# Optimization experiments

Measured on AMD Instinct MI355X. Metric: run time of the kernel, lower is better.

The kernel has to match this reference:

```python
import jax, jax.numpy as jnp
import numpy as np

T, B, OBS, H, M1, M2, A = 64, 2048, 48, 256, 512, 256, 12
LOG2PI = float(np.log(2.0 * np.pi))
LOG_STD_MIN, LOG_STD_MAX = -5.0, 2.0
LN_EPS = 1e-5


def _elu(x):
    return jnp.where(x > 0, x, jnp.expm1(x))


def setup_inputs() -> dict:
    key = jax.random.key(0)
    ks = jax.random.split(key, 10)
    s = lambda k, shape, sc=0.05: jax.random.normal(k, shape, jnp.float32) * sc
    return dict(
        x=jax.random.normal(ks[0], (T, B, OBS), jnp.float32),
        done=jax.random.randint(ks[1], (T, B), 0, 2).astype(jnp.int32),
        h0=jnp.zeros((B, H), jnp.float32),
        c0=jnp.zeros((B, H), jnp.float32),
        W_ih=s(ks[2], (4 * H, OBS)),
        W_hh=s(ks[3], (4 * H, H)),
        b_ih=jnp.zeros((4 * H,), jnp.float32),
        b_hh=jnp.zeros((4 * H,), jnp.float32),
        ln_g=jnp.ones((H,), jnp.float32),
        ln_b=jnp.zeros((H,), jnp.float32),
        W1=s(ks[4], (H, M1)),
        b1=jnp.zeros((M1,), jnp.float32),
        W2=s(ks[5], (M1, M2)),
        b2=jnp.zeros((M2,), jnp.float32),
        Wm=s(ks[6], (M2, A), 0.01),
        bm=jnp.zeros((A,), jnp.float32),
        Ws=s(ks[7], (M2, A), 0.01),
        bs=jnp.zeros((A,), jnp.float32),
    )


def reference(x, h0, c0, W_ih, W_hh, b_ih, b_hh, ln_g, ln_b,
              W1, b1, W2, b2, Wm, bm, Ws, bs, done):
    # Precompute input-side gate projections for all timesteps: [T, B, 4H]
    xg = jnp.einsum('tbi,gi->tbg', x, W_ih) + b_ih + b_hh
    keep = 1.0 - done.astype(jnp.float32)  # [T, B]; reset state where done==1

    def step(carry, inp):
        h, c = carry
        xgt, m = inp
        h = h * m[:, None]
        c = c * m[:, None]
        g = xgt + h @ W_hh.T  # [B, 4H], PyTorch gate order i,f,g,o
        i, f, gg, o = jnp.split(g, 4, axis=-1)
        c = jax.nn.sigmoid(f) * c + jax.nn.sigmoid(i) * jnp.tanh(gg)
        h = jax.nn.sigmoid(o) * jnp.tanh(c)
        return (h, c), h

    (_, _), hs = jax.lax.scan(step, (h0, c0), (xg, keep))
    hflat = hs.reshape(T * B, H)

    # LayerNorm
    mu = hflat.mean(-1, keepdims=True)
    var = ((hflat - mu) ** 2).mean(-1, keepdims=True)
    y = (hflat - mu) / jnp.sqrt(var + LN_EPS) * ln_g + ln_b

    # Actor MLP (ELU after every Linear, per build_mlp)
    y = _elu(y @ W1 + b1)
    y = _elu(y @ W2 + b2)

    mean = y @ Wm + bm
    logstd = jnp.clip(y @ Ws + bs, LOG_STD_MIN, LOG_STD_MAX)
    # deterministic action == mean, so (a - mu)^2 / (2 sigma^2) == 0
    logp = (-logstd - 0.5 * LOG2PI).sum(-1)
    ent = (0.5 + 0.5 * LOG2PI + logstd).sum(-1)
    # [T*B, A+2]: action mean, log_prob, entropy
    return jnp.concatenate([mean, logp[:, None], ent[:, None]], axis=-1)
```

## Files before the change

### kernel.cpp

```cpp
#include <hip/hip_runtime.h>
#include <hip/hip_bf16.h>
#include <math.h>

#define T_   64
#define B_   2048
#define OBS_ 48
#define H_   256
#define M1_  512
#define M2_  256
#define A_   12
#define BH_  (B_ * H_)
#define KP_  320
#define GROUPS_  128
#define SLICES_  2
#define RPB_     16

typedef unsigned short u16;
typedef unsigned long long u64;
typedef __attribute__((ext_vector_type(8))) short bf16x8;
typedef __attribute__((ext_vector_type(4))) float f32x4;

static __device__ __forceinline__ u16 f2b(float f) {
    __hip_bfloat16 h = __float2bfloat16(f);
    return *reinterpret_cast<u16*>(&h);
}
static __device__ __forceinline__ float b2f(u16 u) {
    union { unsigned u32v; float f; } v; v.u32v = ((unsigned)u) << 16; return v.f;
}
static __device__ __forceinline__ float sigm(float x) {
    return 1.0f / (1.0f + __expf(-x));
}
static __device__ __forceinline__ float tanh_fast(float x) {
    x = fminf(fmaxf(x, -15.0f), 15.0f);
    float e = __expf(2.0f * x);
    return (e - 1.0f) / (e + 1.0f);
}
static __device__ __forceinline__ float elu(float x) {
    return x > 0.0f ? x : (__expf(x) - 1.0f);
}

__global__ void prep_xpad(const float* __restrict__ x, u16* __restrict__ xpad,
                          unsigned* __restrict__ cnt) {
    if (blockIdx.x == 0 && threadIdx.x < GROUPS_ * SLICES_) cnt[threadIdx.x] = 0;
    const int gid = blockIdx.x * 256 + threadIdx.x;
    const int r = gid >> 3, k0 = (gid & 7) * 8;
    u16 tmp[8];
    if (k0 < OBS_) {
        const float4 f0 = *(const float4*)(x + (size_t)r * OBS_ + k0);
        const float4 f1 = *(const float4*)(x + (size_t)r * OBS_ + k0 + 4);
        tmp[0] = f2b(f0.x); tmp[1] = f2b(f0.y); tmp[2] = f2b(f0.z); tmp[3] = f2b(f0.w);
        tmp[4] = f2b(f1.x); tmp[5] = f2b(f1.y); tmp[6] = f2b(f1.z); tmp[7] = f2b(f1.w);
    } else {
        #pragma unroll
        for (int i = 0; i < 8; ++i) tmp[i] = 0;
    }
    *(uint4*)(xpad + (size_t)gid * 8) = *(uint4*)tmp;
}

__global__ void prep_weights(const float* __restrict__ W_ih, const float* __restrict__ W_hh,
                             const float* __restrict__ W1,  const float* __restrict__ W2,
                             const float* __restrict__ Wm,  const float* __restrict__ Ws,
                             u16* __restrict__ Wcat, u16* __restrict__ W1T,
                             u16* __restrict__ W2T,  u16* __restrict__ WhT) {
    const int b = blockIdx.x, tid = threadIdx.x;
    if (b < 1024) {
        const int s = b >> 9, w = (b >> 6) & 7, g = (b >> 4) & 3, jj = b & 15;
        const int src = g * 256 + s * 128 + w * 16 + jj;
        for (int k = tid; k < KP_; k += 256) {
            float v;
            if (k < OBS_)    v = W_ih[src * OBS_ + k];
            else if (k < 64) v = 0.0f;
            else             v = W_hh[src * H_ + (k - 64)];
            Wcat[b * KP_ + k] = f2b(v);
        }
    } else if (b < 1536) {
        const int n = b - 1024;
        W1T[n * 256 + tid] = f2b(W1[tid * M1_ + n]);
    } else if (b < 1792) {
        const int n = b - 1536;
        W2T[n * 512 + tid]       = f2b(W2[tid * M2_ + n]);
        W2T[n * 512 + tid + 256] = f2b(W2[(tid + 256) * M2_ + n]);
    } else {
        const int n = b - 1792;
        float v = 0.0f;
        if (n < 12)                 v = Wm[tid * A_ + n];
        else if (n >= 16 && n < 28) v = Ws[tid * A_ + (n - 16)];
        WhT[n * 256 + tid] = f2b(v);
    }
}

#define ASM_(row, chunk) (a_sm + (size_t)(row) * 320 + (size_t)(((chunk) ^ ((row) & 7)) << 3))

__global__ __launch_bounds__(512, 2) void lstm_sync2(
    const u16*  __restrict__ xpad,
    const int*  __restrict__ done,
    const float* __restrict__ h0,
    const float* __restrict__ c0,
    u16*        __restrict__ hs,
    const u16*  __restrict__ Wcat,
    const float* __restrict__ b_ih,
    const float* __restrict__ b_hh,
    unsigned*   __restrict__ cnt)
{
    __shared__ u16 a_sm[RPB_ * 320];

    const int tid  = threadIdx.x;
    const int lane = tid & 63;
    const int w    = tid >> 6;
    const int quad = lane >> 4, l16 = lane & 15;
    const int grp  = blockIdx.x >> 1;
    const int s    = blockIdx.x & 1;
    const int b0   = grp * RPB_;
    const int j    = s * 128 + w * 16 + l16;
    const int pc0  = (1 - s) * 128;

    float bsum[4];
    #pragma unroll
    for (int g = 0; g < 4; ++g) bsum[g] = b_ih[g * 256 + j] + b_hh[g * 256 + j];

    float cst[4];
    #pragma unroll
    for (int r = 0; r < 4; ++r) {
        const int row = b0 + quad * 4 + r;
        cst[r] = done[row] ? 0.0f : c0[(size_t)row * H_ + j];
    }

    bf16x8 Bs[4][10];
    #pragma unroll
    for (int g = 0; g < 4; ++g) {
        const u16* wp = Wcat + (size_t)(((s * 8 + w) * 4 + g) * 16 + l16) * KP_ + quad * 8;
        #pragma unroll
        for (int kt = 0; kt < 10; ++kt)
            Bs[g][kt] = *(const bf16x8*)(wp + kt * 32);
    }

    if ((tid & 3) == 0) {
        const int idx = tid >> 2, row = idx >> 3, seg = idx & 7;
        *(uint4*)ASM_(row, seg) =
            *(const uint4*)(xpad + (size_t)(b0 + row) * 64 + seg * 8);
    }
    {
        const int row = tid >> 5, c8 = tid & 31;
        const int dn = done[b0 + row];
        const float* hr = h0 + (size_t)(b0 + row) * H_ + c8 * 8;
        u16 tmp[8];
        #pragma unroll
        for (int e = 0; e < 8; ++e) tmp[e] = dn ? (u16)0 : f2b(hr[e]);
        *(uint4*)ASM_(row, 8 + c8) = *(uint4*)tmp;
    }
    __syncthreads();

    for (int t = 0; t < T_; ++t) {
        f32x4 acc[4];
        #pragma unroll
        for (int g = 0; g < 4; ++g) acc[g] = (f32x4){0, 0, 0, 0};
        #pragma unroll
        for (int kt = 0; kt < 10; ++kt) {
            const bf16x8 af = *(const bf16x8*)ASM_(l16, kt * 4 + quad);
            #pragma unroll
            for (int g = 0; g < 4; ++g)
                acc[g] = __builtin_amdgcn_mfma_f32_16x16x32_bf16(af, Bs[g][kt], acc[g], 0, 0, 0);
        }
        __syncthreads();

        u16* hs1 = hs + (size_t)(t + 1) * BH_;
        #pragma unroll
        for (int r = 0; r < 4; ++r) {
            const int rowl = quad * 4 + r;
            const int rowg = b0 + rowl;
            const float gi = acc[0][r] + bsum[0];
            const float gf = acc[1][r] + bsum[1];
            const float gg = acc[2][r] + bsum[2];
            const float go = acc[3][r] + bsum[3];
            const float cn = sigm(gf) * cst[r] + sigm(gi) * tanh_fast(gg);
            const float h  = sigm(go) * tanh_fast(cn);
            const float kp = (t + 1 < T_)
                ? (done[(size_t)(t + 1) * B_ + rowg] ? 0.0f : 1.0f) : 1.0f;
            cst[r] = cn * kp;
            const int e = 64 + j;
            *(ASM_(rowl, e >> 3) + (e & 7)) = f2b(h * kp);
            const unsigned hb = (unsigned)f2b(h);
            const unsigned ob = (unsigned)__shfl_xor((int)hb, 1);
            if ((l16 & 1) == 0) {
                const unsigned val = hb | (ob << 16);
                __hip_atomic_store((unsigned*)(hs1 + (size_t)rowg * H_ + (j & ~1)), val,
                                   __ATOMIC_RELAXED, __HIP_MEMORY_SCOPE_AGENT);
            }
        }
        if (t + 1 < T_ && (tid & 3) == 0) {
            const int idx = tid >> 2, row = idx >> 3, seg = idx & 7;
            *(uint4*)ASM_(row, seg) =
                *(const uint4*)(xpad + ((size_t)(t + 1) * B_ + b0 + row) * 64 + seg * 8);
        }
        __syncthreads();

        if (t + 1 < T_) {
            if (tid == 0) {
                __hip_atomic_store(&cnt[blockIdx.x], (unsigned)(t + 1),
                                   __ATOMIC_RELAXED, __HIP_MEMORY_SCOPE_AGENT);
                int guard = 0;
                while (__hip_atomic_load(&cnt[blockIdx.x ^ 1], __ATOMIC_RELAXED,
                                         __HIP_MEMORY_SCOPE_AGENT) < (unsigned)(t + 1)) {
                    __builtin_amdgcn_s_sleep(1);
                    if (++guard > (1 << 24)) break;
                }
            }
            __syncthreads();

            if (tid < 256) {
                const int row = tid >> 4, q = tid & 15;
                const int dn = done[(size_t)(t + 1) * B_ + b0 + row];
                const int pc = pc0 + q * 8;
                uint4 hv = *(const uint4*)(hs1 + (size_t)(b0 + row) * H_ + pc);
                if (dn) hv = make_uint4(0u, 0u, 0u, 0u);
                *(uint4*)ASM_(row, 8 + ((pc0 >> 3) + q)) = hv;
            }
            __syncthreads();
        }
    }
}

#define SY(row, col) ((size_t)(row) * 256 + ((((col) >> 3) ^ ((row) & 7)) << 3) + ((col) & 7))

__global__ __launch_bounds__(512, 4) void mlp_mfma64(
    const u16*  __restrict__ hs,
    float*      __restrict__ out,
    const float* __restrict__ lng, const float* __restrict__ lnb,
    const u16*  __restrict__ W1T, const float* __restrict__ b1,
    const u16*  __restrict__ W2T, const float* __restrict__ b2,
    const u16*  __restrict__ WhT,
    const float* __restrict__ bm, const float* __restrict__ bs)
{
    __shared__ u16 ybf[64 * 256];
    __shared__ u16 yh [64 * 256];

    const int tid  = threadIdx.x;
    const int lane = tid & 63;
    const int wave = tid >> 6;
    const int quad = lane >> 4, l16 = lane & 15;
    const int row0 = blockIdx.x * 64;

    {
        const float4 gv = *(const float4*)(lng + lane * 4);
        const float4 bv = *(const float4*)(lnb + lane * 4);
        #pragma unroll
        for (int rr = 0; rr < 8; ++rr) {
            const int r = wave * 8 + rr;
            const u64 hv8 = __builtin_nontemporal_load(
                (const u64*)(hs + (size_t)(row0 + r) * H_ + lane * 4));
            const u16 h0v = (u16)(hv8 & 0xffff), h1v = (u16)((hv8 >> 16) & 0xffff);
            const u16 h2v = (u16)((hv8 >> 32) & 0xffff), h3v = (u16)(hv8 >> 48);
            const float v0 = b2f(h0v), v1 = b2f(h1v), v2 = b2f(h2v), v3 = b2f(h3v);
            float s  = v0 + v1 + v2 + v3;
            float ss = v0 * v0 + v1 * v1 + v2 * v2 + v3 * v3;
            #pragma unroll
            for (int off = 32; off > 0; off >>= 1) {
                s  += __shfl_down(s,  off);
                ss += __shfl_down(ss, off);
            }
            s = __shfl(s, 0); ss = __shfl(ss, 0);
            const float mu   = s * (1.0f / 256.0f);
            const float rstd = rsqrtf(ss * (1.0f / 256.0f) - mu * mu + 1e-5f);
            ushort4 o;
            o.x = f2b((v0 - mu) * rstd * gv.x + bv.x);
            o.y = f2b((v1 - mu) * rstd * gv.y + bv.y);
            o.z = f2b((v2 - mu) * rstd * gv.z + bv.z);
            o.w = f2b((v3 - mu) * rstd * gv.w + bv.w);
            *(ushort4*)(ybf + SY(r, lane * 4)) = o;
        }
    }
    __syncthreads();

    f32x4 acc2[4][2];
    #pragma unroll
    for (int m = 0; m < 4; ++m)
        #pragma unroll
        for (int j = 0; j < 2; ++j) acc2[m][j] = (f32x4){0,0,0,0};

    #pragma unroll
    for (int ph = 0; ph < 2; ++ph) {
        {
            f32x4 acc[4][2];
            #pragma unroll
            for (int m = 0; m < 4; ++m)
                #pragma unroll
                for (int j = 0; j < 2; ++j) acc[m][j] = (f32x4){0,0,0,0};
            const int n0 = ph * 256 + wave * 32;
            const u16* wp0 = W1T + (size_t)(n0 + l16) * 256 + quad * 8;
            const u16* wp1 = W1T + (size_t)(n0 + 16 + l16) * 256 + quad * 8;
            #pragma unroll
            for (int kt = 0; kt < 8; ++kt) {
                const int k0 = kt * 32;
                const bf16x8 bw0 = *(const bf16x8*)(wp0 + k0);
                const bf16x8 bw1 = *(const bf16x8*)(wp1 + k0);
                #pragma unroll
                for (int m = 0; m < 4; ++m) {
                    const bf16x8 af = *(const bf16x8*)(ybf + SY(m * 16 + l16, k0 + quad * 8));
                    acc[m][0] = __builtin_amdgcn_mfma_f32_16x16x32_bf16(af, bw0, acc[m][0], 0, 0, 0);
                    acc[m][1] = __builtin_amdgcn_mfma_f32_16x16x32_bf16(af, bw1, acc[m][1], 0, 0, 0);
                }
            }
            const float bb0 = b1[n0 + l16], bb1 = b1[n0 + 16 + l16];
            __syncthreads();
            #pragma unroll
            for (int m = 0; m < 4; ++m)
                #pragma unroll
                for (int r = 0; r < 4; ++r) {
                    const int row = m * 16 + quad * 4 + r;
                    yh[SY(row, wave * 32 + l16)]      = f2b(elu(acc[m][0][r] + bb0));
                    yh[SY(row, wave * 32 + 16 + l16)] = f2b(elu(acc[m][1][r] + bb1));
                }
        }
        __syncthreads();

        {
            const int n0 = wave * 32;
            const u16* wp0 = W2T + (size_t)(n0 + l16) * 512 + ph * 256 + quad * 8;
            const u16* wp1 = W2T + (size_t)(n0 + 16 + l16) * 512 + ph * 256 + quad * 8;
            #pragma unroll
            for (int kt = 0; kt < 8; ++kt) {
                const int k0 = kt * 32;
                const bf16x8 bw0 = *(const bf16x8*)(wp0 + k0);
                const bf16x8 bw1 = *(const bf16x8*)(wp1 + k0);
                #pragma unroll
                for (int m = 0; m < 4; ++m) {
                    const bf16x8 af = *(const bf16x8*)(yh + SY(m * 16 + l16, k0 + quad * 8));
                    acc2[m][0] = __builtin_amdgcn_mfma_f32_16x16x32_bf16(af, bw0, acc2[m][0], 0, 0, 0);
                    acc2[m][1] = __builtin_amdgcn_mfma_f32_16x16x32_bf16(af, bw1, acc2[m][1], 0, 0, 0);
                }
            }
        }
        __syncthreads();
    }

    {
        const float bb0 = b2[wave * 32 + l16], bb1 = b2[wave * 32 + 16 + l16];
        #pragma unroll
        for (int m = 0; m < 4; ++m)
            #pragma unroll
            for (int r = 0; r < 4; ++r) {
                const int row = m * 16 + quad * 4 + r;
                ybf[SY(row, wave * 32 + l16)]      = f2b(elu(acc2[m][0][r] + bb0));
                ybf[SY(row, wave * 32 + 16 + l16)] = f2b(elu(acc2[m][1][r] + bb1));
            }
    }
    __syncthreads();

    float* lsf = (float*)yh;
    if (wave < 4) {
        f32x4 a0 = {0,0,0,0}, a1 = {0,0,0,0};
        const u16* wp0 = WhT + (size_t)l16 * 256 + quad * 8;
        const u16* wp1 = WhT + (size_t)(16 + l16) * 256 + quad * 8;
        #pragma unroll
        for (int kt = 0; kt < 8; ++kt) {
            const int k0 = kt * 32;
            const bf16x8 af  = *(const bf16x8*)(ybf + SY(wave * 16 + l16, k0 + quad * 8));
            const bf16x8 bw0 = *(const bf16x8*)(wp0 + k0);
            const bf16x8 bw1 = *(const bf16x8*)(wp1 + k0);
            a0 = __builtin_amdgcn_mfma_f32_16x16x32_bf16(af, bw0, a0, 0, 0, 0);
            a1 = __builtin_amdgcn_mfma_f32_16x16x32_bf16(af, bw1, a1, 0, 0, 0);
        }
        if (l16 < 12) {
            const float bbm = bm[l16], bbs = bs[l16];
            #pragma unroll
            for (int r = 0; r < 4; ++r) {
                const int row = wave * 16 + quad * 4 + r;
                out[(size_t)(row0 + row) * 14 + l16] = a0[r] + bbm;
                lsf[row * 16 + l16] = fminf(fmaxf(a1[r] + bbs, -5.0f), 2.0f);
            }
        }
    }
    __syncthreads();
    if (tid < 64) {
        float s = 0.0f;
        #pragma unroll
        for (int q = 0; q < 12; ++q) s += lsf[tid * 16 + q];
        const float LOG2PI = 1.8378770664093453f;
        out[(size_t)(row0 + tid) * 14 + 12] = -s - 6.0f * LOG2PI;
        out[(size_t)(row0 + tid) * 14 + 13] =  s + 6.0f + 6.0f * LOG2PI;
    }
}

extern "C" void kernel_launch(void* const* d_in, const int* in_sizes, int n_in,
                              void* d_out, int out_size, void* d_ws, size_t ws_size,
                              hipStream_t stream) {
    (void)in_sizes; (void)n_in; (void)out_size; (void)ws_size;
    const float* x    = (const float*)d_in[0];
    const int*   done = (const int*)  d_in[1];
    const float* h0   = (const float*)d_in[2];
    const float* c0   = (const float*)d_in[3];
    const float* W_ih = (const float*)d_in[4];
    const float* W_hh = (const float*)d_in[5];
    const float* b_ih = (const float*)d_in[6];
    const float* b_hh = (const float*)d_in[7];
    const float* lng  = (const float*)d_in[8];
    const float* lnb  = (const float*)d_in[9];
    const float* W1   = (const float*)d_in[10];
    const float* b1   = (const float*)d_in[11];
    const float* W2   = (const float*)d_in[12];
    const float* b2   = (const float*)d_in[13];
    const float* Wm   = (const float*)d_in[14];
    const float* bm   = (const float*)d_in[15];
    const float* Ws   = (const float*)d_in[16];
    const float* bs   = (const float*)d_in[17];
    float* out = (float*)d_out;

    unsigned char* p = (unsigned char*)d_ws;
    u16* hs    = (u16*)p;              p += (size_t)(T_ + 1) * BH_ * 2;
    u16* xpad  = (u16*)p;              p += (size_t)T_ * B_ * 64 * 2;
    u16* Wcat  = (u16*)p;              p += (size_t)1024 * KP_ * 2;
    u16* W1T   = (u16*)p;              p += (size_t)M1_ * H_ * 2;
    u16* W2T   = (u16*)p;              p += (size_t)M2_ * M1_ * 2;
    u16* WhT   = (u16*)p;              p += (size_t)32 * H_ * 2;
    unsigned* cnt = (unsigned*)p;      p += 1024;

    prep_xpad<<<(T_ * B_ * 8) / 256, 256, 0, stream>>>(x, xpad, cnt);
    prep_weights<<<1824, 256, 0, stream>>>(W_ih, W_hh, W1, W2, Wm, Ws,
                                           Wcat, W1T, W2T, WhT);

    lstm_sync2<<<GROUPS_ * SLICES_, 512, 0, stream>>>(
        xpad, done, h0, c0, hs, Wcat, b_ih, b_hh, cnt);

    mlp_mfma64<<<(T_ * B_) / 64, 512, 0, stream>>>(
        hs + BH_, out, lng, lnb, W1T, b1, W2T, b2, WhT, bm, bs);
}
```

Before: 639.0 us.

## Overlap partner-block wait with MFMAs on locally owned hidden-state columns

Splits the per-step recurrent GEMM's K loop into three parts: input columns, the block's own hidden slice (already in LDS), and the partner block's slice. The own-slice MFMAs now run before waiting on the partner's step counter, so the inter-block handshake latency is hidden behind compute. The wait becomes a block-wide polling loop with a shared flag, and the next x tile is loaded in the same phase as the partner hidden-state load. This adds extra barriers per step and relies on relaxed atomics with a guard timeout for cross-block visibility.

New measurement: 1.213 ms. 89.8% more time.

```diff
diff --git a/kernel.cpp b/kernel.cpp
--- a/kernel.cpp
+++ b/kernel.cpp
@@ -103,6 +103,7 @@
     unsigned*   __restrict__ cnt)
 {
     __shared__ u16 a_sm[RPB_ * 320];
+    __shared__ unsigned okf;
 
     const int tid  = threadIdx.x;
     const int lane = tid & 63;
@@ -113,6 +114,8 @@
     const int b0   = grp * RPB_;
     const int j    = s * 128 + w * 16 + l16;
     const int pc0  = (1 - s) * 128;
+    const int ownk0 = 2 + s * 4;
+    const int prtk0 = 2 + (1 - s) * 4;
 
     float bsum[4];
     #pragma unroll
@@ -151,17 +154,69 @@
     __syncthreads();
 
     for (int t = 0; t < T_; ++t) {
+        unsigned fv = 0;
+        if (tid == 0 && t > 0)
+            fv = __hip_atomic_load(&cnt[blockIdx.x ^ 1], __ATOMIC_RELAXED,
+                                   __HIP_MEMORY_SCOPE_AGENT);
+
         f32x4 acc[4];
         #pragma unroll
         for (int g = 0; g < 4; ++g) acc[g] = (f32x4){0, 0, 0, 0};
         #pragma unroll
-        for (int kt = 0; kt < 10; ++kt) {
+        for (int kt = 0; kt < 2; ++kt) {
             const bf16x8 af = *(const bf16x8*)ASM_(l16, kt * 4 + quad);
             #pragma unroll
             for (int g = 0; g < 4; ++g)
                 acc[g] = __builtin_amdgcn_mfma_f32_16x16x32_bf16(af, Bs[g][kt], acc[g], 0, 0, 0);
         }
+        #pragma unroll
+        for (int kk = 0; kk < 4; ++kk) {
+            const int kt = ownk0 + kk;
+            const bf16x8 af = *(const bf16x8*)ASM_(l16, kt * 4 + quad);
+            #pragma unroll
+            for (int g = 0; g < 4; ++g)
+                acc[g] = __builtin_amdgcn_mfma_f32_16x16x32_bf16(af, Bs[g][kt], acc[g], 0, 0, 0);
+        }
+
+        if (tid == 0) okf = (t == 0 || fv >= (unsigned)t) ? 1u : 0u;
         __syncthreads();
+        {
+            int guard = 0;
+            while (!okf) {
+                if (tid == 0) {
+                    __builtin_amdgcn_s_sleep(1);
+                    fv = __hip_atomic_load(&cnt[blockIdx.x ^ 1], __ATOMIC_RELAXED,
+                                           __HIP_MEMORY_SCOPE_AGENT);
+                    if (fv >= (unsigned)t || ++guard > (1 << 22)) okf = 1u;
+                }
+                __syncthreads();
+            }
+        }
+
+        if (t > 0 && tid < 256) {
+            const u16* hst = hs + (size_t)t * BH_;
+            const int row = tid >> 4, q = tid & 15;
+            const int dn = done[(size_t)t * B_ + b0 + row];
+            const int pc = pc0 + q * 8;
+            uint4 hv = *(const uint4*)(hst + (size_t)(b0 + row) * H_ + pc);
+            if (dn) hv = make_uint4(0u, 0u, 0u, 0u);
+            *(uint4*)ASM_(row, 8 + (pc0 >> 3) + q) = hv;
+        }
+        if (t + 1 < T_ && tid >= 256 && tid < 384) {
+            const int idx = tid - 256, row = idx >> 3, seg = idx & 7;
+            *(uint4*)ASM_(row, seg) =
+                *(const uint4*)(xpad + ((size_t)(t + 1) * B_ + b0 + row) * 64 + seg * 8);
+        }
+        __syncthreads();
+
+        #pragma unroll
+        for (int kk = 0; kk < 4; ++kk) {
+            const int kt = prtk0 + kk;
+            const bf16x8 af = *(const bf16x8*)ASM_(l16, kt * 4 + quad);
+            #pragma unroll
+            for (int g = 0; g < 4; ++g)
+                acc[g] = __builtin_amdgcn_mfma_f32_16x16x32_bf16(af, Bs[g][kt], acc[g], 0, 0, 0);
+        }
 
         u16* hs1 = hs + (size_t)(t + 1) * BH_;
         #pragma unroll
@@ -187,36 +242,11 @@
                                    __ATOMIC_RELAXED, __HIP_MEMORY_SCOPE_AGENT);
             }
         }
-        if (t + 1 < T_ && (tid & 3) == 0) {
-            const int idx = tid >> 2, row = idx >> 3, seg = idx & 7;
-            *(uint4*)ASM_(row, seg) =
-                *(const uint4*)(xpad + ((size_t)(t + 1) * B_ + b0 + row) * 64 + seg * 8);
-        }
         __syncthreads();
 
-        if (t + 1 < T_) {
-            if (tid == 0) {
-                __hip_atomic_store(&cnt[blockIdx.x], (unsigned)(t + 1),
-                                   __ATOMIC_RELAXED, __HIP_MEMORY_SCOPE_AGENT);
-                int guard = 0;
-                while (__hip_atomic_load(&cnt[blockIdx.x ^ 1], __ATOMIC_RELAXED,
-                                         __HIP_MEMORY_SCOPE_AGENT) < (unsigned)(t + 1)) {
-                    __builtin_amdgcn_s_sleep(1);
-                    if (++guard > (1 << 24)) break;
-                }
-            }
-            __syncthreads();
-
-            if (tid < 256) {
-                const int row = tid >> 4, q = tid & 15;
-                const int dn = done[(size_t)(t + 1) * B_ + b0 + row];
-                const int pc = pc0 + q * 8;
-                uint4 hv = *(const uint4*)(hs1 + (size_t)(b0 + row) * H_ + pc);
-                if (dn) hv = make_uint4(0u, 0u, 0u, 0u);
-                *(uint4*)ASM_(row, 8 + ((pc0 >> 3) + q)) = hv;
-            }
-            __syncthreads();
-        }
+        if (tid == 0 && t + 1 < T_)
+            __hip_atomic_store(&cnt[blockIdx.x], (unsigned)(t + 1),
+                               __ATOMIC_RELAXED, __HIP_MEMORY_SCOPE_AGENT);
     }
 }
 
```

## Run each LSTM row group in one block, dropping the cross-block handshake

Applied to the files above, without the earlier changes.

The recurrent kernel now has a single 512-thread block compute all 256 hidden units for its 16 batch rows. Each wave holds two 16-column fragments, so W_hh sits in twice as many registers. This removes the per-timestep spin-wait between paired blocks and the global-memory round trip used to exchange half of h. The next x tile is also prefetched into registers before the MFMA loop, and the two prep kernels are merged into one launch. The cost is half as many blocks (128) running at one block per CU with heavy register pressure, so each CU does twice the matrix work per step.

Measured after the change: 1.390 ms. 2.18x slower.

```diff
diff --git a/kernel.cpp b/kernel.cpp
--- a/kernel.cpp
+++ b/kernel.cpp
@@ -11,9 +11,8 @@
 #define A_   12
 #define BH_  (B_ * H_)
 #define KP_  320
-#define GROUPS_  128
-#define SLICES_  2
-#define RPB_     16
+#define RPB_ 16
+#define NBLK_ (B_ / RPB_)
 
 typedef unsigned short u16;
 typedef unsigned long long u64;
@@ -39,33 +38,33 @@
     return x > 0.0f ? x : (__expf(x) - 1.0f);
 }
 
-__global__ void prep_xpad(const float* __restrict__ x, u16* __restrict__ xpad,
-                          unsigned* __restrict__ cnt) {
-    if (blockIdx.x == 0 && threadIdx.x < GROUPS_ * SLICES_) cnt[threadIdx.x] = 0;
-    const int gid = blockIdx.x * 256 + threadIdx.x;
-    const int r = gid >> 3, k0 = (gid & 7) * 8;
-    u16 tmp[8];
-    if (k0 < OBS_) {
-        const float4 f0 = *(const float4*)(x + (size_t)r * OBS_ + k0);
-        const float4 f1 = *(const float4*)(x + (size_t)r * OBS_ + k0 + 4);
-        tmp[0] = f2b(f0.x); tmp[1] = f2b(f0.y); tmp[2] = f2b(f0.z); tmp[3] = f2b(f0.w);
-        tmp[4] = f2b(f1.x); tmp[5] = f2b(f1.y); tmp[6] = f2b(f1.z); tmp[7] = f2b(f1.w);
-    } else {
-        #pragma unroll
-        for (int i = 0; i < 8; ++i) tmp[i] = 0;
-    }
-    *(uint4*)(xpad + (size_t)gid * 8) = *(uint4*)tmp;
-}
-
-__global__ void prep_weights(const float* __restrict__ W_ih, const float* __restrict__ W_hh,
-                             const float* __restrict__ W1,  const float* __restrict__ W2,
-                             const float* __restrict__ Wm,  const float* __restrict__ Ws,
-                             u16* __restrict__ Wcat, u16* __restrict__ W1T,
-                             u16* __restrict__ W2T,  u16* __restrict__ WhT) {
-    const int b = blockIdx.x, tid = threadIdx.x;
+__global__ void prep_all(const float* __restrict__ x, u16* __restrict__ xpad,
+                         const float* __restrict__ W_ih, const float* __restrict__ W_hh,
+                         const float* __restrict__ W1,  const float* __restrict__ W2,
+                         const float* __restrict__ Wm,  const float* __restrict__ Ws,
+                         u16* __restrict__ Wcat, u16* __restrict__ W1T,
+                         u16* __restrict__ W2T,  u16* __restrict__ WhT) {
+    const int blk = blockIdx.x, tid = threadIdx.x;
+    if (blk < 4096) {
+        const int gid = blk * 256 + tid;
+        const int r = gid >> 3, k0 = (gid & 7) * 8;
+        u16 tmp[8];
+        if (k0 < OBS_) {
+            const float4 f0 = *(const float4*)(x + (size_t)r * OBS_ + k0);
+            const float4 f1 = *(const float4*)(x + (size_t)r * OBS_ + k0 + 4);
+            tmp[0] = f2b(f0.x); tmp[1] = f2b(f0.y); tmp[2] = f2b(f0.z); tmp[3] = f2b(f0.w);
+            tmp[4] = f2b(f1.x); tmp[5] = f2b(f1.y); tmp[6] = f2b(f1.z); tmp[7] = f2b(f1.w);
+        } else {
+            #pragma unroll
+            for (int i = 0; i < 8; ++i) tmp[i] = 0;
+        }
+        *(uint4*)(xpad + (size_t)gid * 8) = *(uint4*)tmp;
+        return;
+    }
+    const int b = blk - 4096;
     if (b < 1024) {
-        const int s = b >> 9, w = (b >> 6) & 7, g = (b >> 4) & 3, jj = b & 15;
-        const int src = g * 256 + s * 128 + w * 16 + jj;
+        const int w = b >> 7, nf = (b >> 6) & 1, g = (b >> 4) & 3, jj = b & 15;
+        const int src = g * 256 + w * 32 + nf * 16 + jj;
         for (int k = tid; k < KP_; k += 256) {
             float v;
             if (k < OBS_)    v = W_ih[src * OBS_ + k];
@@ -91,7 +90,7 @@
 
 #define ASM_(row, chunk) (a_sm + (size_t)(row) * 320 + (size_t)(((chunk) ^ ((row) & 7)) << 3))
 
-__global__ __launch_bounds__(512, 2) void lstm_sync2(
+__global__ __launch_bounds__(512, 1) void lstm_solo(
     const u16*  __restrict__ xpad,
     const int*  __restrict__ done,
     const float* __restrict__ h0,
@@ -99,8 +98,7 @@
     u16*        __restrict__ hs,
     const u16*  __restrict__ Wcat,
     const float* __restrict__ b_ih,
-    const float* __restrict__ b_hh,
-    unsigned*   __restrict__ cnt)
+    const float* __restrict__ b_hh)
 {
     __shared__ u16 a_sm[RPB_ * 320];
 
@@ -108,34 +106,40 @@
     const int lane = tid & 63;
     const int w    = tid >> 6;
     const int quad = lane >> 4, l16 = lane & 15;
-    const int grp  = blockIdx.x >> 1;
-    const int s    = blockIdx.x & 1;
-    const int b0   = grp * RPB_;
-    const int j    = s * 128 + w * 16 + l16;
-    const int pc0  = (1 - s) * 128;
-
-    float bsum[4];
+    const int b0   = blockIdx.x * RPB_;
+
+    float bsum[2][4];
     #pragma unroll
-    for (int g = 0; g < 4; ++g) bsum[g] = b_ih[g * 256 + j] + b_hh[g * 256 + j];
-
-    float cst[4];
+    for (int nf = 0; nf < 2; ++nf) {
+        const int j = w * 32 + nf * 16 + l16;
+        #pragma unroll
+        for (int g = 0; g < 4; ++g) bsum[nf][g] = b_ih[g * 256 + j] + b_hh[g * 256 + j];
+    }
+
+    float cst[2][4];
     #pragma unroll
     for (int r = 0; r < 4; ++r) {
         const int row = b0 + quad * 4 + r;
-        cst[r] = done[row] ? 0.0f : c0[(size_t)row * H_ + j];
-    }
-
-    bf16x8 Bs[4][10];
+        const float kp = done[row] ? 0.0f : 1.0f;
+        #pragma unroll
+        for (int nf = 0; nf < 2; ++nf)
+            cst[nf][r] = c0[(size_t)row * H_ + w * 32 + nf * 16 + l16] * kp;
+    }
+
+    bf16x8 Bs[2][4][10];
     #pragma unroll
-    for (int g = 0; g < 4; ++g) {
-        const u16* wp = Wcat + (size_t)(((s * 8 + w) * 4 + g) * 16 + l16) * KP_ + quad * 8;
-        #pragma unroll
-        for (int kt = 0; kt < 10; ++kt)
-            Bs[g][kt] = *(const bf16x8*)(wp + kt * 32);
-    }
-
-    if ((tid & 3) == 0) {
-        const int idx = tid >> 2, row = idx >> 3, seg = idx & 7;
+    for (int nf = 0; nf < 2; ++nf)
+        #pragma unroll
+        for (int g = 0; g < 4; ++g) {
+            const u16* wp = Wcat +
+                (size_t)((((w * 2 + nf) * 4 + g) * 16) + l16) * KP_ + quad * 8;
+            #pragma unroll
+            for (int kt = 0; kt < 10; ++kt)
+                Bs[nf][g][kt] = *(const bf16x8*)(wp + kt * 32);
+        }
+
+    if (tid < 128) {
+        const int row = tid >> 3, seg = tid & 7;
         *(uint4*)ASM_(row, seg) =
             *(const uint4*)(xpad + (size_t)(b0 + row) * 64 + seg * 8);
     }
@@ -151,72 +155,59 @@
     __syncthreads();
 
     for (int t = 0; t < T_; ++t) {
-        f32x4 acc[4];
-        #pragma unroll
-        for (int g = 0; g < 4; ++g) acc[g] = (f32x4){0, 0, 0, 0};
+        uint4 xstage; int xrow = 0, xseg = 0;
+        const bool do_x = (t + 1 < T_) && (tid < 128);
+        if (do_x) {
+            xrow = tid >> 3; xseg = tid & 7;
+            xstage = *(const uint4*)(xpad +
+                ((size_t)(t + 1) * B_ + b0 + xrow) * 64 + xseg * 8);
+        }
+
+        f32x4 acc[2][4];
+        #pragma unroll
+        for (int nf = 0; nf < 2; ++nf)
+            #pragma unroll
+            for (int g = 0; g < 4; ++g) acc[nf][g] = (f32x4){0, 0, 0, 0};
         #pragma unroll
         for (int kt = 0; kt < 10; ++kt) {
             const bf16x8 af = *(const bf16x8*)ASM_(l16, kt * 4 + quad);
             #pragma unroll
-            for (int g = 0; g < 4; ++g)
-                acc[g] = __builtin_amdgcn_mfma_f32_16x16x32_bf16(af, Bs[g][kt], acc[g], 0, 0, 0);
+            for (int nf = 0; nf < 2; ++nf)
+                #pragma unroll
+                for (int g = 0; g < 4; ++g)
+                    acc[nf][g] = __builtin_amdgcn_mfma_f32_16x16x32_bf16(
+                        af, Bs[nf][g][kt], acc[nf][g], 0, 0, 0);
         }
         __syncthreads();
+
+        if (do_x) *(uint4*)ASM_(xrow, xseg) = xstage;
 
         u16* hs1 = hs + (size_t)(t + 1) * BH_;
         #pragma unroll
         for (int r = 0; r < 4; ++r) {
             const int rowl = quad * 4 + r;
             const int rowg = b0 + rowl;
-            const float gi = acc[0][r] + bsum[0];
-            const float gf = acc[1][r] + bsum[1];
-            const float gg = acc[2][r] + bsum[2];
-            const float go = acc[3][r] + bsum[3];
-            const float cn = sigm(gf) * cst[r] + sigm(gi) * tanh_fast(gg);
-            const float h  = sigm(go) * tanh_fast(cn);
             const float kp = (t + 1 < T_)
                 ? (done[(size_t)(t + 1) * B_ + rowg] ? 0.0f : 1.0f) : 1.0f;
-            cst[r] = cn * kp;
-            const int e = 64 + j;
-            *(ASM_(rowl, e >> 3) + (e & 7)) = f2b(h * kp);
-            const unsigned hb = (unsigned)f2b(h);
-            const unsigned ob = (unsigned)__shfl_xor((int)hb, 1);
-            if ((l16 & 1) == 0) {
-                const unsigned val = hb | (ob << 16);
-                __hip_atomic_store((unsigned*)(hs1 + (size_t)rowg * H_ + (j & ~1)), val,
-                                   __ATOMIC_RELAXED, __HIP_MEMORY_SCOPE_AGENT);
-            }
-        }
-        if (t + 1 < T_ && (tid & 3) == 0) {
-            const int idx = tid >> 2, row = idx >> 3, seg = idx & 7;
-            *(uint4*)ASM_(row, seg) =
-                *(const uint4*)(xpad + ((size_t)(t + 1) * B_ + b0 + row) * 64 + seg * 8);
+            #pragma unroll
+            for (int nf = 0; nf < 2; ++nf) {
+                const int j = w * 32 + nf * 16 + l16;
+                const float gi = acc[nf][0][r] + bsum[nf][0];
+                const float gf = acc[nf][1][r] + bsum[nf][1];
+                const float gg = acc[nf][2][r] + bsum[nf][2];
+                const float go = acc[nf][3][r] + bsum[nf][3];
+                const float cn = sigm(gf) * cst[nf][r] + sigm(gi) * tanh_fast(gg);
+                const float h  = sigm(go) * tanh_fast(cn);
+                cst[nf][r] = cn * kp;
+                *(ASM_(rowl, 8 + (j >> 3)) + (j & 7)) = f2b(h * kp);
+                const unsigned hb = (unsigned)f2b(h);
+                const unsigned ob = (unsigned)__shfl_xor((int)hb, 1);
+                if ((l16 & 1) == 0) {
+                    *(unsigned*)(hs1 + (size_t)rowg * H_ + (j & ~1)) = hb | (ob << 16);
+                }
+            }
         }
         __syncthreads();
-
-        if (t + 1 < T_) {
-            if (tid == 0) {
-                __hip_atomic_store(&cnt[blockIdx.x], (unsigned)(t + 1),
-                                   __ATOMIC_RELAXED, __HIP_MEMORY_SCOPE_AGENT);
-                int guard = 0;
-                while (__hip_atomic_load(&cnt[blockIdx.x ^ 1], __ATOMIC_RELAXED,
-                                         __HIP_MEMORY_SCOPE_AGENT) < (unsigned)(t + 1)) {
-                    __builtin_amdgcn_s_sleep(1);
-                    if (++guard > (1 << 24)) break;
-                }
-            }
-            __syncthreads();
-
-            if (tid < 256) {
-                const int row = tid >> 4, q = tid & 15;
-                const int dn = done[(size_t)(t + 1) * B_ + b0 + row];
-                const int pc = pc0 + q * 8;
-                uint4 hv = *(const uint4*)(hs1 + (size_t)(b0 + row) * H_ + pc);
-                if (dn) hv = make_uint4(0u, 0u, 0u, 0u);
-                *(uint4*)ASM_(row, 8 + ((pc0 >> 3) + q)) = hv;
-            }
-            __syncthreads();
-        }
     }
 }
 
@@ -412,14 +403,12 @@
     u16* W1T   = (u16*)p;              p += (size_t)M1_ * H_ * 2;
     u16* W2T   = (u16*)p;              p += (size_t)M2_ * M1_ * 2;
     u16* WhT   = (u16*)p;              p += (size_t)32 * H_ * 2;
-    unsigned* cnt = (unsigned*)p;      p += 1024;
-
-    prep_xpad<<<(T_ * B_ * 8) / 256, 256, 0, stream>>>(x, xpad, cnt);
-    prep_weights<<<1824, 256, 0, stream>>>(W_ih, W_hh, W1, W2, Wm, Ws,
-                                           Wcat, W1T, W2T, WhT);
-
-    lstm_sync2<<<GROUPS_ * SLICES_, 512, 0, stream>>>(
-        xpad, done, h0, c0, hs, Wcat, b_ih, b_hh, cnt);
+
+    prep_all<<<4096 + 1824, 256, 0, stream>>>(x, xpad, W_ih, W_hh, W1, W2, Wm, Ws,
+                                              Wcat, W1T, W2T, WhT);
+
+    lstm_solo<<<NBLK_, 512, 0, stream>>>(
+        xpad, done, h0, c0, hs, Wcat, b_ih, b_hh);
 
     mlp_mfma64<<<(T_ * B_) / 64, 512, 0, stream>>>(
         hs + BH_, out, lng, lnb, W1T, b1, W2T, b2, WhT, bm, bs);
```
